# Optimization experiments

Measured on AMD Instinct MI355X. Metric: run time of the kernel, lower is better.

Reference implementation:

```python
import jax, jax.numpy as jnp
import numpy as np

B, C, H, W = 128, 1024, 16, 12
CI = 512              # inter_channels = in_channels // 2
EPS = 1e-4            # module's self.eps for std normalization
BN_EPS = 1e-5         # torch BatchNorm2d default eps (eval mode, running stats)


def setup_inputs() -> dict:
    key = jax.random.key(0)
    ks = jax.random.split(key, 8)
    s_in = 1.0 / np.sqrt(C)
    s_192 = 1.0 / np.sqrt(192)
    s_64 = 1.0 / np.sqrt(64)
    return {
        "x": jax.random.normal(ks[0], (B, C, H, W), jnp.float32),
        "theta_w": jax.random.normal(ks[1], (CI, C), jnp.float32) * s_in,
        "theta_b": jax.random.normal(ks[2], (CI,), jnp.float32) * s_in,
        "phi_w": jax.random.normal(ks[3], (CI, C), jnp.float32) * s_in,
        "phi_b": jax.random.normal(ks[4], (CI,), jnp.float32) * s_in,
        "m1_w": jax.random.normal(ks[5], (64, H * W), jnp.float32) * s_192,
        "m1_b": jax.random.normal(ks[6], (64,), jnp.float32) * s_192,
        "bn_g": jnp.ones((64,), jnp.float32),
        "bn_b": jnp.zeros((64,), jnp.float32),
        "bn_m": jnp.zeros((64,), jnp.float32),
        "bn_v": jnp.ones((64,), jnp.float32),
        "m2_w": jax.random.normal(ks[7], (1, 64), jnp.float32) * s_64,
        "m2_b": jnp.zeros((1,), jnp.float32),
    }


def _conv1x1(x, w, b):
    # x: (B, Cin, H, W), w: (Cout, Cin) -> (B, Cout, H, W)
    return jnp.einsum("bchw,oc->bohw", x, w) + b[None, :, None, None]


def reference(x, theta_w, theta_b, phi_w, phi_b, m1_w, m1_b,
              bn_g, bn_b, bn_m, bn_v, m2_w, m2_b):
    b, c, h, w = x.shape
    hw = h * w

    # theta/phi 1x1 conv projections -> (B, CI, HW)
    theta = _conv1x1(x, theta_w, theta_b).reshape(b, CI, hw)
    phi = _conv1x1(x, phi_w, phi_b).reshape(b, CI, hw)

    # theta_x: (B, HW, CI), z-score over channel axis (torch.std unbiased, ddof=1)
    theta_x = jnp.transpose(theta, (0, 2, 1))
    theta_x = theta_x - jnp.mean(theta_x, axis=2, keepdims=True)
    theta_x = theta_x / (jnp.std(theta_x, axis=2, keepdims=True, ddof=1) + EPS)

    # phi_x: (B, CI, HW), z-score over channel axis (dim 1)
    phi_x = phi - jnp.mean(phi, axis=1, keepdims=True)
    phi_x = phi_x / (jnp.std(phi_x, axis=1, keepdims=True, ddof=1) + EPS)

    # correlation: (B, HW, HW), divided by phi_x.size(1) == CI
    f = jnp.einsum("bnc,bcm->bnm", theta_x, phi_x) / CI

    # transpose then view as (B, HW, H, W) image of correlation maps
    mc = jnp.transpose(f, (0, 2, 1)).reshape(b, hw, h, w)

    # spatial_mask_summary: conv1x1(192->64) -> BN (eval) -> ReLU -> conv1x1(64->1)
    t = _conv1x1(mc, m1_w, m1_b)
    t = (t - bn_m[None, :, None, None]) * (
        bn_g[None, :, None, None] / jnp.sqrt(bn_v + BN_EPS)[None, :, None, None]
    ) + bn_b[None, :, None, None]
    t = jax.nn.relu(t)
    mask = jax.nn.sigmoid(_conv1x1(t, m2_w, m2_b))  # (B, 1, H, W)

    # sigmoid-gated residual
    return x + mask * x
```

## Files before the change

kernel.cpp:

```cpp
#include <hip/hip_runtime.h>

#define B_N 128
#define C_N 1024
#define HW_N 192
#define CI_N 512
#define MROWS (B_N * HW_N)

typedef short bf16x8 __attribute__((ext_vector_type(8)));
typedef float f32x4 __attribute__((ext_vector_type(4)));
typedef unsigned short us4 __attribute__((ext_vector_type(4)));
typedef unsigned short us8 __attribute__((ext_vector_type(8)));

__device__ __forceinline__ unsigned short f2bf(float f){
    unsigned int u = __builtin_bit_cast(unsigned int, f);
    u += 0x7fffu + ((u >> 16) & 1u);
    return (unsigned short)(u >> 16);
}
__device__ __forceinline__ float bf2f(unsigned short h){
    unsigned int u = ((unsigned int)h) << 16;
    return __builtin_bit_cast(float, u);
}
__device__ __forceinline__ void gload_lds16(const void* g, void* l){
    __builtin_amdgcn_global_load_lds(
        (const __attribute__((address_space(1))) unsigned int*)g,
        (__attribute__((address_space(3))) unsigned int*)l, 16, 0, 0);
}

__global__ __launch_bounds__(256) void k_prep(const float* __restrict__ x,
                                              unsigned short* __restrict__ xbT,
                                              const float* __restrict__ tw, const float* __restrict__ tb,
                                              const float* __restrict__ pw, const float* __restrict__ pb,
                                              const float* __restrict__ m1w,
                                              unsigned short* __restrict__ Wc, float* __restrict__ bias,
                                              unsigned short* __restrict__ w1b){
    __shared__ float tile[64][37];
    int b  = blockIdx.z;
    int c0 = blockIdx.y * 64;
    int n0 = blockIdx.x * 32;
    int t  = threadIdx.x;

    int fid = ((blockIdx.z * gridDim.y + blockIdx.y) * gridDim.x + blockIdx.x) * 256 + t;
    if (fid < 1024 * 1024){
        int o = fid >> 10, c = fid & 1023;
        float v = (o < 512) ? tw[(size_t)o * 1024 + c] : pw[(size_t)(o - 512) * 1024 + c];
        Wc[fid] = f2bf(v);
        if (fid < 1024) bias[fid] = (fid < 512) ? tb[fid] : pb[fid - 512];
        if (fid < 64 * HW_N) w1b[fid] = f2bf(m1w[fid]);
    }

    const float* xp = x + (size_t)b * C_N * HW_N;
    int cr = t >> 3;
    int nw = (t & 7) * 4;
    #pragma unroll
    for (int i = 0; i < 2; ++i){
        float4 v = *(const float4*)(xp + (size_t)(c0 + cr + 32 * i) * HW_N + n0 + nw);
        tile[cr + 32 * i][nw + 0] = v.x;
        tile[cr + 32 * i][nw + 1] = v.y;
        tile[cr + 32 * i][nw + 2] = v.z;
        tile[cr + 32 * i][nw + 3] = v.w;
    }
    __syncthreads();
    int nl = t >> 3;
    int j  = t & 7;
    us8 pk;
    #pragma unroll
    for (int e = 0; e < 8; ++e)
        pk[e] = f2bf(tile[j * 8 + e][nl]);
    *(us8*)(xbT + (size_t)(b * HW_N + n0 + nl) * C_N + c0 + j * 8) = pk;
}

__global__ __launch_bounds__(256, 3) void k_gemm1(const unsigned short* __restrict__ Wc,
                                               const float* __restrict__ bias,
                                               const unsigned short* __restrict__ xbT,
                                               unsigned short* __restrict__ TPt,
                                               float2* __restrict__ part){
    __shared__ __align__(16) unsigned short lW[128 * 64];
    __shared__ __align__(16) unsigned short lX[128 * 64];
    int bid  = blockIdx.x;
    int xcd  = bid & 7;
    int slot = bid >> 3;
    int mb = xcd * 24 + (slot >> 3);
    int nb = slot & 7;
    int tid = threadIdx.x, lane = tid & 63, wave = tid >> 6;
    int wr = wave >> 1, wc = wave & 1;
    int fr = lane & 15, fg = lane >> 4;

    const unsigned short* Wg = Wc  + (size_t)(nb * 128) * C_N;
    const unsigned short* Xg = xbT + (size_t)(mb * 128) * C_N;

    int row0 = tid >> 3;
    int su   = tid & 7;
    int gsw  = (su ^ (row0 & 7)) * 8;
    const unsigned short* wsrc = Wg + (size_t)row0 * C_N + gsw;
    const unsigned short* xsrc = Xg + (size_t)row0 * C_N + gsw;

    f32x4 acc[4][4];
    f32x4 zero = {0.f, 0.f, 0.f, 0.f};
    #pragma unroll
    for (int i = 0; i < 4; ++i)
        #pragma unroll
        for (int j = 0; j < 4; ++j)
            acc[i][j] = zero;

    for (int k0 = 0; k0 < C_N; k0 += 64){
        __syncthreads();
        #pragma unroll
        for (int i = 0; i < 4; ++i){
            gload_lds16(wsrc + (size_t)(32 * i) * C_N + k0, (char*)lW + tid * 16 + i * 4096);
            gload_lds16(xsrc + (size_t)(32 * i) * C_N + k0, (char*)lX + tid * 16 + i * 4096);
        }
        __syncthreads();

        #pragma unroll
        for (int kk = 0; kk < 2; ++kk){
            bf16x8 wf[4], xf[4];
            #pragma unroll
            for (int j = 0; j < 4; ++j){
                int row = wc * 64 + j * 16 + fr;
                int un  = (kk * 4 + fg) ^ (row & 7);
                wf[j] = *(const bf16x8*)((char*)lW + row * 128 + un * 16);
            }
            #pragma unroll
            for (int i = 0; i < 4; ++i){
                int row = wr * 64 + i * 16 + fr;
                int un  = (kk * 4 + fg) ^ (row & 7);
                xf[i] = *(const bf16x8*)((char*)lX + row * 128 + un * 16);
            }
            #pragma unroll
            for (int i = 0; i < 4; ++i)
                #pragma unroll
                for (int j = 0; j < 4; ++j)
                    acc[i][j] = __builtin_amdgcn_mfma_f32_16x16x32_bf16(wf[j], xf[i], acc[i][j], 0, 0, 0);
        }
    }

    float s[4] = {0.f,0.f,0.f,0.f}, q[4] = {0.f,0.f,0.f,0.f};
    #pragma unroll
    for (int i = 0; i < 4; ++i){
        int n = mb * 128 + wr * 64 + i * 16 + fr;
        #pragma unroll
        for (int j = 0; j < 4; ++j){
            int o0 = nb * 128 + wc * 64 + j * 16 + fg * 4;
            float4 b4 = *(const float4*)(bias + o0);
            float v0 = acc[i][j][0] + b4.x;
            float v1 = acc[i][j][1] + b4.y;
            float v2 = acc[i][j][2] + b4.z;
            float v3 = acc[i][j][3] + b4.w;
            s[i] += v0 + v1 + v2 + v3;
            q[i] += v0*v0 + v1*v1 + v2*v2 + v3*v3;
            us4 pk;
            pk[0] = f2bf(v0); pk[1] = f2bf(v1); pk[2] = f2bf(v2); pk[3] = f2bf(v3);
            *(us4*)(TPt + (size_t)n * 1024 + o0) = pk;
        }
    }
    #pragma unroll
    for (int i = 0; i < 4; ++i){
        s[i] += __shfl_xor(s[i], 16); s[i] += __shfl_xor(s[i], 32);
        q[i] += __shfl_xor(q[i], 16); q[i] += __shfl_xor(q[i], 32);
    }
    if (lane < 16){
        int chunk = nb * 2 + wc;
        #pragma unroll
        for (int i = 0; i < 4; ++i){
            int n = mb * 128 + wr * 64 + i * 16 + fr;
            part[(size_t)n * 16 + chunk] = make_float2(s[i], q[i]);
        }
    }
}

__global__ __launch_bounds__(256) void k_gemm2m(const unsigned short* __restrict__ TPt,
        const float2* __restrict__ part,
        const unsigned short* __restrict__ w1b, const float* __restrict__ m1b,
        const float* __restrict__ bng, const float* __restrict__ bnb,
        const float* __restrict__ bnm, const float* __restrict__ bnv,
        const float* __restrict__ m2w, const float* __restrict__ m2b,
        float* __restrict__ mask){
    __shared__ __align__(16) unsigned short lT[64 * 64];
    __shared__ __align__(16) unsigned short lP[192 * 64];
    __shared__ __align__(16) unsigned short lF[64 * 200];
    int tn = blockIdx.x;
    int b  = blockIdx.y;
    int tid = threadIdx.x, lane = tid & 63, wave = tid >> 6;
    int wr = wave >> 1, wc = wave & 1;
    int fr = lane & 15, fg = lane >> 4;

    int rbase = tid >> 3;
    int su    = tid & 7;
    const unsigned short* src[8];
    float2 st[8];
    unsigned short* dst[8];
    #pragma unroll
    for (int i = 0; i < 8; ++i){
        int srow = rbase + 32 * i;
        int swz  = (su ^ (srow & 7)) * 16;
        const float2* pp;
        if (i < 2){
            int gn = b * HW_N + tn * 64 + srow;
            src[i] = TPt + (size_t)gn * 1024 + su * 8;
            pp     = part + (size_t)gn * 16;
            dst[i] = (unsigned short*)((char*)lT + srow * 128 + swz);
        } else {
            int prow = srow - 64;
            int gm = b * HW_N + prow;
            src[i] = TPt + (size_t)gm * 1024 + 512 + su * 8;
            pp     = part + (size_t)gm * 16 + 8;
            dst[i] = (unsigned short*)((char*)lP + prow * 128 + swz);
        }
        float S = 0.f, Q = 0.f;
        #pragma unroll
        for (int k = 0; k < 8; ++k){ float2 v = pp[k]; S += v.x; Q += v.y; }
        float mean = S * (1.f / 512.f);
        float var  = (Q - 512.f * mean * mean) * (1.f / 511.f);
        st[i] = make_float2(mean, 1.f / (sqrtf(fmaxf(var, 0.f)) + 1e-4f));
    }

    f32x4 acc[3][2][2];
    f32x4 zero = {0.f, 0.f, 0.f, 0.f};
    #pragma unroll
    for (int t = 0; t < 3; ++t)
        #pragma unroll
        for (int i = 0; i < 2; ++i)
            #pragma unroll
            for (int j = 0; j < 2; ++j)
                acc[t][i][j] = zero;

    for (int k0 = 0; k0 < CI_N; k0 += 64){
        bf16x8 nv[8];
        #pragma unroll
        for (int i = 0; i < 8; ++i){
            bf16x8 v = *(const bf16x8*)(src[i] + k0);
            #pragma unroll
            for (int e = 0; e < 8; ++e)
                nv[i][e] = (short)f2bf((bf2f((unsigned short)v[e]) - st[i].x) * st[i].y);
        }
        __syncthreads();
        #pragma unroll
        for (int i = 0; i < 8; ++i)
            *(bf16x8*)dst[i] = nv[i];
        __syncthreads();

        #pragma unroll
        for (int kk = 0; kk < 2; ++kk){
            bf16x8 tf[2];
            #pragma unroll
            for (int i = 0; i < 2; ++i){
                int row = wr * 32 + i * 16 + fr;
                int un  = (kk * 4 + fg) ^ (row & 7);
                tf[i] = *(const bf16x8*)((char*)lT + row * 128 + un * 16);
            }
            #pragma unroll
            for (int t = 0; t < 3; ++t){
                #pragma unroll
                for (int j = 0; j < 2; ++j){
                    int row = t * 64 + wc * 32 + j * 16 + fr;
                    int un  = (kk * 4 + fg) ^ (row & 7);
                    bf16x8 pf = *(const bf16x8*)((char*)lP + row * 128 + un * 16);
                    #pragma unroll
                    for (int i = 0; i < 2; ++i)
                        acc[t][i][j] = __builtin_amdgcn_mfma_f32_16x16x32_bf16(pf, tf[i], acc[t][i][j], 0, 0, 0);
                }
            }
        }
    }

    __syncthreads();
    #pragma unroll
    for (int t = 0; t < 3; ++t)
        #pragma unroll
        for (int i = 0; i < 2; ++i){
            int n = wr * 32 + i * 16 + fr;
            #pragma unroll
            for (int j = 0; j < 2; ++j){
                int m0 = t * 64 + wc * 32 + j * 16 + fg * 4;
                us4 pk;
                #pragma unroll
                for (int r = 0; r < 4; ++r)
                    pk[r] = f2bf(acc[t][i][j][r] * (1.0f / 512.0f));
                *(us4*)((char*)lF + ((size_t)n * 200 + m0) * 2) = pk;
            }
        }
    __syncthreads();

    f32x4 macc[4];
    #pragma unroll
    for (int j = 0; j < 4; ++j) macc[j] = zero;
    #pragma unroll
    for (int kk = 0; kk < 6; ++kk){
        bf16x8 af = *(const bf16x8*)((char*)lF + ((size_t)(wave * 16 + fr) * 200 + kk * 32 + fg * 8) * 2);
        #pragma unroll
        for (int j = 0; j < 4; ++j){
            bf16x8 bfv = *(const bf16x8*)(w1b + (size_t)(j * 16 + fr) * HW_N + kk * 32 + fg * 8);
            macc[j] = __builtin_amdgcn_mfma_f32_16x16x32_bf16(af, bfv, macc[j], 0, 0, 0);
        }
    }
    float sc[4], sh[4], bb[4], w2v[4];
    #pragma unroll
    for (int j = 0; j < 4; ++j){
        int o = j * 16 + fr;
        float s = bng[o] * rsqrtf(bnv[o] + 1e-5f);
        sc[j] = s;
        sh[j] = bnb[o] - bnm[o] * s;
        bb[j] = m1b[o];
        w2v[j] = m2w[o];
    }
    float mb2 = m2b[0];
    #pragma unroll
    for (int r = 0; r < 4; ++r){
        float y = 0.f;
        #pragma unroll
        for (int j = 0; j < 4; ++j){
            float t = fmaxf((macc[j][r] + bb[j]) * sc[j] + sh[j], 0.f);
            y += t * w2v[j];
        }
        y += __shfl_xor(y, 1);
        y += __shfl_xor(y, 2);
        y += __shfl_xor(y, 4);
        y += __shfl_xor(y, 8);
        if (fr == 0)
            mask[(size_t)b * HW_N + tn * 64 + wave * 16 + fg * 4 + r] =
                1.f + 1.f / (1.f + __expf(-(y + mb2)));
    }
}

__global__ __launch_bounds__(256) void k_apply(const float* __restrict__ x,
                                               const float* __restrict__ mask,
                                               float* __restrict__ out){
    size_t i4 = (size_t)blockIdx.x * 256 + threadIdx.x;
    size_t e  = i4 * 4;
    float4 v = ((const float4*)x)[i4];
    size_t n = e % HW_N;
    size_t b = e / ((size_t)C_N * HW_N);
    const float* mk = mask + b * HW_N + n;
    float4 o;
    o.x = v.x * mk[0];
    o.y = v.y * mk[1];
    o.z = v.z * mk[2];
    o.w = v.w * mk[3];
    ((float4*)out)[i4] = o;
}

extern "C" void kernel_launch(void* const* d_in, const int* in_sizes, int n_in,
                              void* d_out, int out_size, void* d_ws, size_t ws_size,
                              hipStream_t stream){
    (void)in_sizes; (void)n_in; (void)out_size; (void)ws_size;
    const float* x   = (const float*)d_in[0];
    const float* tw  = (const float*)d_in[1];
    const float* tb  = (const float*)d_in[2];
    const float* pw  = (const float*)d_in[3];
    const float* pb  = (const float*)d_in[4];
    const float* m1w = (const float*)d_in[5];
    const float* m1b = (const float*)d_in[6];
    const float* bng = (const float*)d_in[7];
    const float* bnb = (const float*)d_in[8];
    const float* bnm = (const float*)d_in[9];
    const float* bnv = (const float*)d_in[10];
    const float* m2w = (const float*)d_in[11];
    const float* m2b = (const float*)d_in[12];
    float* out = (float*)d_out;

    char* ws = (char*)d_ws;
    size_t off = 0;
    unsigned short* xbT = (unsigned short*)(ws + off); off += (size_t)MROWS * C_N * 2;
    unsigned short* Wc  = (unsigned short*)(ws + off); off += (size_t)1024 * 1024 * 2;
    float* bias         = (float*)(ws + off);          off += 4096;
    unsigned short* TPt = (unsigned short*)(ws + off); off += (size_t)MROWS * 1024 * 2;
    float* mask         = (float*)(ws + off);          off += (size_t)MROWS * 4;
    unsigned short* w1b = (unsigned short*)(ws + off); off += (size_t)64 * HW_N * 2;
    off = (off + 255) & ~(size_t)255;
    float2* part        = (float2*)(ws + off);         off += (size_t)MROWS * 16 * 8;

    k_prep<<<dim3(6, 16, B_N), 256, 0, stream>>>(x, xbT, tw, tb, pw, pb, m1w, Wc, bias, w1b);
    k_gemm1<<<dim3(1536), 256, 0, stream>>>(Wc, bias, xbT, TPt, part);
    k_gemm2m<<<dim3(3, B_N), 256, 0, stream>>>(TPt, part, w1b, m1b, bng, bnb, bnm, bnv, m2w, m2b, mask);
    k_apply<<<dim3(MROWS * C_N / 4 / 256), 256, 0, stream>>>(x, mask, out);
}
```

Baseline: 161.8 us.

## Fold z-score normalization into correlation epilogue and load tiles directly to LDS

```diff
diff --git a/kernel.cpp b/kernel.cpp
--- a/kernel.cpp
+++ b/kernel.cpp
@@ -178,41 +178,34 @@
     __shared__ __align__(16) unsigned short lT[64 * 64];
     __shared__ __align__(16) unsigned short lP[192 * 64];
     __shared__ __align__(16) unsigned short lF[64 * 200];
+    __shared__ float2 stT[64];
+    __shared__ float2 stP[192];
     int tn = blockIdx.x;
     int b  = blockIdx.y;
     int tid = threadIdx.x, lane = tid & 63, wave = tid >> 6;
     int wr = wave >> 1, wc = wave & 1;
     int fr = lane & 15, fg = lane >> 4;
 
-    int rbase = tid >> 3;
-    int su    = tid & 7;
-    const unsigned short* src[8];
-    float2 st[8];
-    unsigned short* dst[8];
-    #pragma unroll
-    for (int i = 0; i < 8; ++i){
-        int srow = rbase + 32 * i;
-        int swz  = (su ^ (srow & 7)) * 16;
+    {
         const float2* pp;
-        if (i < 2){
-            int gn = b * HW_N + tn * 64 + srow;
-            src[i] = TPt + (size_t)gn * 1024 + su * 8;
-            pp     = part + (size_t)gn * 16;
-            dst[i] = (unsigned short*)((char*)lT + srow * 128 + swz);
-        } else {
-            int prow = srow - 64;
-            int gm = b * HW_N + prow;
-            src[i] = TPt + (size_t)gm * 1024 + 512 + su * 8;
-            pp     = part + (size_t)gm * 16 + 8;
-            dst[i] = (unsigned short*)((char*)lP + prow * 128 + swz);
-        }
+        if (tid < 64)
+            pp = part + (size_t)(b * HW_N + tn * 64 + tid) * 16;
+        else
+            pp = part + (size_t)(b * HW_N + (tid - 64)) * 16 + 8;
         float S = 0.f, Q = 0.f;
         #pragma unroll
         for (int k = 0; k < 8; ++k){ float2 v = pp[k]; S += v.x; Q += v.y; }
         float mean = S * (1.f / 512.f);
         float var  = (Q - 512.f * mean * mean) * (1.f / 511.f);
-        st[i] = make_float2(mean, 1.f / (sqrtf(fmaxf(var, 0.f)) + 1e-4f));
-    }
+        float2 r = make_float2(mean, 1.f / (sqrtf(fmaxf(var, 0.f)) + 1e-4f));
+        if (tid < 64) stT[tid] = r; else stP[tid - 64] = r;
+    }
+
+    int row0 = tid >> 3;
+    int su   = tid & 7;
+    int gsw  = (su ^ (row0 & 7)) * 8;
+    const unsigned short* tsrc = TPt + (size_t)(b * HW_N + tn * 64 + row0) * 1024 + gsw;
+    const unsigned short* psrc = TPt + (size_t)(b * HW_N + row0) * 1024 + 512 + gsw;
 
     f32x4 acc[3][2][2];
     f32x4 zero = {0.f, 0.f, 0.f, 0.f};
@@ -225,18 +218,12 @@
                 acc[t][i][j] = zero;
 
     for (int k0 = 0; k0 < CI_N; k0 += 64){
-        bf16x8 nv[8];
-        #pragma unroll
-        for (int i = 0; i < 8; ++i){
-            bf16x8 v = *(const bf16x8*)(src[i] + k0);
-            #pragma unroll
-            for (int e = 0; e < 8; ++e)
-                nv[i][e] = (short)f2bf((bf2f((unsigned short)v[e]) - st[i].x) * st[i].y);
-        }
         __syncthreads();
-        #pragma unroll
-        for (int i = 0; i < 8; ++i)
-            *(bf16x8*)dst[i] = nv[i];
+        gload_lds16(tsrc + k0,                      (char*)lT + tid * 16);
+        gload_lds16(tsrc + (size_t)32 * 1024 + k0,  (char*)lT + tid * 16 + 4096);
+        #pragma unroll
+        for (int i = 0; i < 6; ++i)
+            gload_lds16(psrc + (size_t)(32 * i) * 1024 + k0, (char*)lP + tid * 16 + i * 4096);
         __syncthreads();
 
         #pragma unroll
@@ -268,15 +255,19 @@
     for (int t = 0; t < 3; ++t)
         #pragma unroll
         for (int i = 0; i < 2; ++i){
-            int n = wr * 32 + i * 16 + fr;
+            int nl = wr * 32 + i * 16 + fr;
+            float2 sn = stT[nl];
             #pragma unroll
             for (int j = 0; j < 2; ++j){
                 int m0 = t * 64 + wc * 32 + j * 16 + fg * 4;
                 us4 pk;
                 #pragma unroll
-                for (int r = 0; r < 4; ++r)
-                    pk[r] = f2bf(acc[t][i][j][r] * (1.0f / 512.0f));
-                *(us4*)((char*)lF + ((size_t)n * 200 + m0) * 2) = pk;
+                for (int r = 0; r < 4; ++r){
+                    float2 sm = stP[m0 + r];
+                    float F = (acc[t][i][j][r] - 512.f * sn.x * sm.x) * sn.y * sm.y * (1.0f / 512.0f);
+                    pk[r] = f2bf(F);
+                }
+                *(us4*)((char*)lF + ((size_t)nl * 200 + m0) * 2) = pk;
             }
         }
     __syncthreads();
```

After: 144.8 us. 10.5% less time.
